# Kernel optimization log

Hardware: AMD Instinct MI355X
Metric: run time of the kernel (lower is better)

## Reference

```python
import jax, jax.numpy as jnp
import numpy as np

EPS = 1e-12
LAMBDA = 0.5  # kernel['lambda'] for the binary kernel

D, H, Z = 3072, 1024, 32
BS, NN = 128, 32


def setup_inputs() -> dict:
    key = jax.random.key(0)
    ks = jax.random.split(key, 16)
    sc = lambda fan_in: 1.0 / np.sqrt(fan_in)
    inp = {
        "x_c": jax.random.normal(ks[0], (BS, D), jnp.float32),
        "x_nn": jax.random.normal(ks[1], (BS, NN, D), jnp.float32),
        # encoder params: D -> H -> H -> Z
        "We1": jax.random.normal(ks[2], (D, H), jnp.float32) * sc(D),
        "be1": jnp.zeros((H,), jnp.float32),
        "We2": jax.random.normal(ks[3], (H, H), jnp.float32) * sc(H),
        "be2": jnp.zeros((H,), jnp.float32),
        "We3": jax.random.normal(ks[4], (H, Z), jnp.float32) * sc(H),
        "be3": jnp.zeros((Z,), jnp.float32),
        # decoder params: Z -> H -> H -> D
        "Wd1": jax.random.normal(ks[5], (Z, H), jnp.float32) * sc(Z),
        "bd1": jnp.zeros((H,), jnp.float32),
        "Wd2": jax.random.normal(ks[6], (H, H), jnp.float32) * sc(H),
        "bd2": jnp.zeros((H,), jnp.float32),
        "Wd3": jax.random.normal(ks[7], (H, D), jnp.float32) * sc(H),
        "bd3": jnp.zeros((D,), jnp.float32),
    }
    return inp


def _mlp(x, W1, b1, W2, b2, W3, b3):
    h = jax.nn.relu(x @ W1 + b1)
    h = jax.nn.relu(h @ W2 + b2)
    return h @ W3 + b3


def reference(x_c, x_nn, We1, be1, We2, be2, We3, be3,
              Wd1, bd1, Wd2, bd2, Wd3, bd3):
    bs, num_nn, dim = x_nn.shape

    enc = lambda x: _mlp(x, We1, be1, We2, be2, We3, be3)
    dec = lambda z: _mlp(z, Wd1, bd1, Wd2, bd2, Wd3, bd3)

    z_c = enc(x_c)                                   # (bs, Z)
    z_dim = z_c.shape[1]
    z_nn = enc(x_nn.reshape(-1, dim)).reshape(bs, num_nn, z_dim)

    recon = dec(z_c)                                 # (bs, D)
    dz = z_nn - z_c[:, None, :]                      # (bs, nn, Z)
    v = dz.reshape(-1, z_dim)                        # (bs*nn, Z)
    inputs = jnp.broadcast_to(z_c[:, None, :], (bs, num_nn, z_dim)).reshape(-1, z_dim)

    # approx_order == 2: Jacobian-vector and Hessian-bilinear (dz^T H dz) via nested jvp
    jac_fn = lambda z: jax.jvp(dec, (z,), (v,))[1]   # J(z) dz, (bs*nn, D)
    jac, hess = jax.jvp(jac_fn, (inputs,), (v,))     # each (bs*nn, D)

    n_recon = recon[:, None, :] + (jac + 0.5 * hess).reshape(bs, num_nn, dim)

    n_loss = jnp.sum((x_nn - n_recon) ** 2, axis=2)  # ||.||^2, (bs, nn)

    # binary kernel: 1 where neighbor differs from center, lambda where identical
    dist = jnp.linalg.norm(x_c[:, None, :] - x_nn, axis=2)
    weights = jnp.where(dist > EPS, 1.0, LAMBDA)

    loss = jnp.mean(weights * n_loss)
    return loss
```

## Files before the change

### kernel.cpp

```cpp
#include <hip/hip_runtime.h>
#include <math.h>

#define D_DIM 3072
#define H_DIM 1024
#define Z_DIM 32
#define BATCH 128
#define NNEI 32
#define NROWS (BATCH * NNEI)
#define MENC (NROWS + BATCH)

typedef __attribute__((ext_vector_type(8))) short short8;
typedef __attribute__((ext_vector_type(4))) float f32x4;
typedef unsigned short ushortT;

__device__ __forceinline__ unsigned short f2bf(float f) {
  union { float f; unsigned int u; } v; v.f = f;
  unsigned int r = v.u + 0x7FFFu + ((v.u >> 16) & 1u);
  return (unsigned short)(r >> 16);
}
__device__ __forceinline__ float bf2f(unsigned short b) {
  union { unsigned int u; float f; } v; v.u = ((unsigned int)b) << 16;
  return v.f;
}

enum { EP_RELU = 0, EP_BIAS = 1, EP_LOSS = 2 };

template <int MODE, int TN>
__global__ __launch_bounds__(256) __attribute__((amdgpu_waves_per_eu(1, 2)))
void gemm_sb(
    const ushortT* __restrict__ A, const ushortT* __restrict__ BT,
    const float* __restrict__ bias, ushortT* __restrict__ C,
    int M, int N, int K,
    const ushortT* __restrict__ xa,
    const float* __restrict__ wrow,
    float* __restrict__ out) {
  constexpr int NF = TN / 32;

  __shared__ __align__(16) ushortT As[4096];
  __shared__ __align__(16) ushortT Bs[TN * 32];

  const int t = threadIdx.x;
  const int wave = t >> 6;
  const int lane = t & 63;
  const int quad = lane >> 4;
  const int lm = lane & 15;
  const int bm = blockIdx.y * 128;
  const int bn = blockIdx.x * TN;
  const int wr = (wave >> 1) * 64;
  const int wc = (wave & 1) * (TN / 2);

  f32x4 acc[4][NF];
#pragma unroll
  for (int i = 0; i < 4; ++i)
#pragma unroll
    for (int j = 0; j < NF; ++j) acc[i][j] = (f32x4)0.f;

  const int a_r0 = (t >> 6) * 16 + (t & 15);
  const int a_q8 = ((t >> 4) & 3) * 8;
  const ushortT* ga0 = A + (size_t)(bm + a_r0) * K + a_q8;
  const ushortT* ga1 = ga0 + (size_t)64 * K;
  ushortT* wa0 = As + t * 8;
  ushortT* wa1 = As + t * 8 + 2048;

  const ushortT* gb0 = nullptr;
  const ushortT* gb1 = nullptr;
  ushortT* wb0 = nullptr;
  ushortT* wb1 = nullptr;
  bool bact = true;
  if (TN == 128) {
    gb0 = BT + (size_t)(bn + a_r0) * K + a_q8;
    gb1 = gb0 + (size_t)64 * K;
    wb0 = Bs + t * 8;
    wb1 = Bs + t * 8 + 2048;
  } else {
    bact = (t < 128);
    const int s = t & 127;
    const int b_r = (s >> 6) * 16 + (s & 15);
    const int b_q8 = ((s >> 4) & 3) * 8;
    gb0 = BT + (size_t)(bn + b_r) * K + b_q8;
    wb0 = Bs + s * 8;
  }

  uint4 ra0 = *(const uint4*)ga0;
  uint4 ra1 = *(const uint4*)ga1;
  uint4 rb0 = {0, 0, 0, 0};
  uint4 rb1 = {0, 0, 0, 0};
  if (bact) rb0 = *(const uint4*)gb0;
  if (TN == 128) rb1 = *(const uint4*)gb1;
  ga0 += 32; ga1 += 32;
  gb0 += 32;
  if (TN == 128) gb1 += 32;

  const ushortT* arp = As + (wr >> 4) * 512 + lane * 8;
  const ushortT* brp = Bs + (wc >> 4) * 512 + lane * 8;

  for (int k0 = 0; k0 < K; k0 += 32) {
    __syncthreads();
    *(uint4*)wa0 = ra0;
    *(uint4*)wa1 = ra1;
    if (bact) *(uint4*)wb0 = rb0;
    if (TN == 128) *(uint4*)wb1 = rb1;
    __syncthreads();

    if (k0 + 32 < K) {
      ra0 = *(const uint4*)ga0;
      ra1 = *(const uint4*)ga1;
      if (bact) rb0 = *(const uint4*)gb0;
      if (TN == 128) rb1 = *(const uint4*)gb1;
      ga0 += 32; ga1 += 32;
      gb0 += 32;
      if (TN == 128) gb1 += 32;
    }

    short8 af[4], bf[NF];
#pragma unroll
    for (int mt = 0; mt < 4; ++mt) af[mt] = *(const short8*)(arp + mt * 512);
#pragma unroll
    for (int nt = 0; nt < NF; ++nt) bf[nt] = *(const short8*)(brp + nt * 512);
#pragma unroll
    for (int mt = 0; mt < 4; ++mt)
#pragma unroll
      for (int nt = 0; nt < NF; ++nt)
        acc[mt][nt] = __builtin_amdgcn_mfma_f32_16x16x32_bf16(af[mt], bf[nt], acc[mt][nt], 0, 0, 0);
  }

  if (MODE == EP_LOSS) {
    __shared__ float red[256];
    float lsum = 0.f;
#pragma unroll
    for (int mt = 0; mt < 4; ++mt) {
#pragma unroll
      for (int r = 0; r < 4; ++r) {
        const int row = bm + wr + mt * 16 + quad * 4 + r;
        const float w = wrow[row];
        const ushortT* xr = xa + (size_t)row * N;
        float rs = 0.f;
#pragma unroll
        for (int nt = 0; nt < NF; ++nt) {
          const int col = bn + wc + nt * 16 + lm;
          const float d = bf2f(xr[col]) - (acc[mt][nt][r] + bias[col]);
          rs = fmaf(d, d, rs);
        }
        lsum = fmaf(w, rs, lsum);
      }
    }
    __syncthreads();
    red[t] = lsum;
    __syncthreads();
    for (int st = 128; st > 0; st >>= 1) {
      if (t < st) red[t] += red[t + st];
      __syncthreads();
    }
    if (t == 0) atomicAdd(out, red[0] * (1.0f / (float)NROWS));
  } else {
#pragma unroll
    for (int mt = 0; mt < 4; ++mt)
#pragma unroll
      for (int r = 0; r < 4; ++r) {
        const int row = bm + wr + mt * 16 + quad * 4 + r;
#pragma unroll
        for (int nt = 0; nt < NF; ++nt) {
          const int col = bn + wc + nt * 16 + lm;
          float v = acc[mt][nt][r] + bias[col];
          if (MODE == EP_RELU) v = fmaxf(v, 0.f);
          C[(size_t)row * N + col] = f2bf(v);
        }
      }
  }
}

__global__ __launch_bounds__(256) void mask_apply(
    const ushortT* __restrict__ U, ushortT* __restrict__ outp) {
  const int i4 = (blockIdx.x * 256 + threadIdx.x) * 4;
  const int r = i4 >> 10;
  const int c = i4 & 1023;
  ushort4 u = *(const ushort4*)(U + i4);
  ushort4 o;
  if (r < NROWS) {
    const ushort4 m = *(const ushort4*)(U + (((size_t)(NROWS + (r >> 5))) << 10) + c);
    o.x = ((short)m.x > 0) ? u.x : 0;
    o.y = ((short)m.y > 0) ? u.y : 0;
    o.z = ((short)m.z > 0) ? u.z : 0;
    o.w = ((short)m.w > 0) ? u.w : 0;
  } else {
    o.x = ((short)u.x > 0) ? u.x : 0;
    o.y = ((short)u.y > 0) ? u.y : 0;
    o.z = ((short)u.z > 0) ? u.z : 0;
    o.w = ((short)u.w > 0) ? u.w : 0;
  }
  *(ushort4*)(outp + i4) = o;
}

__global__ __launch_bounds__(256) void prep_kernel(
    const float* __restrict__ x_c, const float* __restrict__ x_nn,
    ushortT* __restrict__ A_enc, float* __restrict__ wbuf, float* __restrict__ out) {
  const int i = blockIdx.x;
  const int t = threadIdx.x;
  if (i < NROWS) {
    const float* src = x_nn + (size_t)i * D_DIM;
    const float* ctr = x_c + (size_t)(i >> 5) * D_DIM;
    ushortT* dst = A_enc + (size_t)i * D_DIM;
    float s = 0.f;
    for (int d = t * 4; d < D_DIM; d += 1024) {
      const float4 v = *(const float4*)(src + d);
      const float4 c = *(const float4*)(ctr + d);
      ushort4 o;
      o.x = f2bf(v.x); o.y = f2bf(v.y); o.z = f2bf(v.z); o.w = f2bf(v.w);
      *(ushort4*)(dst + d) = o;
      const float dx = v.x - c.x, dy = v.y - c.y, dz = v.z - c.z, dw = v.w - c.w;
      s += dx * dx + dy * dy + dz * dz + dw * dw;
    }
    __shared__ float red[256];
    red[t] = s;
    __syncthreads();
    for (int st = 128; st > 0; st >>= 1) {
      if (t < st) red[t] += red[t + st];
      __syncthreads();
    }
    if (t == 0) {
      wbuf[i] = (red[0] > 1e-24f) ? 1.0f : 0.5f;
      if (i == 0) out[0] = 0.f;
    }
  } else {
    const int r = i - NROWS;
    const float* src = x_c + (size_t)r * D_DIM;
    ushortT* dst = A_enc + (size_t)i * D_DIM;
    for (int d = t * 4; d < D_DIM; d += 1024) {
      const float4 v = *(const float4*)(src + d);
      ushort4 o;
      o.x = f2bf(v.x); o.y = f2bf(v.y); o.z = f2bf(v.z); o.w = f2bf(v.w);
      *(ushort4*)(dst + d) = o;
    }
  }
}

__global__ __launch_bounds__(256) void trans_all(
    const float* __restrict__ We1, const float* __restrict__ We2,
    const float* __restrict__ We3, const float* __restrict__ Wd1,
    const float* __restrict__ Wd2, const float* __restrict__ Wd3,
    ushortT* __restrict__ We1T, ushortT* __restrict__ We2T,
    ushortT* __restrict__ We3T, ushortT* __restrict__ Wd1T,
    ushortT* __restrict__ Wd2T, ushortT* __restrict__ Wd3T) {
  const int b = blockIdx.x;
  const float* W; ushortT* WT; int K, N, loc;
  if (b < 3072)      { W = We1; WT = We1T; K = 3072; N = 1024; loc = b; }
  else if (b < 4096) { W = We2; WT = We2T; K = 1024; N = 1024; loc = b - 3072; }
  else if (b < 4128) { W = We3; WT = We3T; K = 1024; N = 32;   loc = b - 4096; }
  else if (b < 4160) { W = Wd1; WT = Wd1T; K = 32;   N = 1024; loc = b - 4128; }
  else if (b < 5184) { W = Wd2; WT = Wd2T; K = 1024; N = 1024; loc = b - 4160; }
  else               { W = Wd3; WT = Wd3T; K = 1024; N = 3072; loc = b - 5184; }
  const int ntiles = N >> 5;
  const int n0 = (loc % ntiles) * 32;
  const int k0 = (loc / ntiles) * 32;
  __shared__ float tile[32][33];
  const int tx = threadIdx.x & 31;
  const int ty = threadIdx.x >> 5;
  for (int i = ty; i < 32; i += 8)
    tile[i][tx] = W[(size_t)(k0 + i) * N + n0 + tx];
  __syncthreads();
  for (int i = ty; i < 32; i += 8)
    WT[(size_t)(n0 + i) * K + k0 + tx] = f2bf(tile[tx][i]);
}

extern "C" void kernel_launch(void* const* d_in, const int* in_sizes, int n_in,
                              void* d_out, int out_size, void* d_ws, size_t ws_size,
                              hipStream_t stream) {
  const float* x_c = (const float*)d_in[0];
  const float* x_nn = (const float*)d_in[1];
  const float* We1 = (const float*)d_in[2];
  const float* be1 = (const float*)d_in[3];
  const float* We2 = (const float*)d_in[4];
  const float* be2 = (const float*)d_in[5];
  const float* We3 = (const float*)d_in[6];
  const float* be3 = (const float*)d_in[7];
  const float* Wd1 = (const float*)d_in[8];
  const float* bd1 = (const float*)d_in[9];
  const float* Wd2 = (const float*)d_in[10];
  const float* bd2 = (const float*)d_in[11];
  const float* Wd3 = (const float*)d_in[12];
  const float* bd3 = (const float*)d_in[13];
  float* out = (float*)d_out;

  char* p = (char*)d_ws;
  auto alloc = [&](size_t bytes) {
    char* r = p;
    p += (bytes + 255) & ~(size_t)255;
    return r;
  };
  ushortT* We1T = (ushortT*)alloc((size_t)H_DIM * D_DIM * 2);
  ushortT* We2T = (ushortT*)alloc((size_t)H_DIM * H_DIM * 2);
  ushortT* We3T = (ushortT*)alloc((size_t)Z_DIM * H_DIM * 2);
  ushortT* Wd1T = (ushortT*)alloc((size_t)H_DIM * Z_DIM * 2);
  ushortT* Wd2T = (ushortT*)alloc((size_t)H_DIM * H_DIM * 2);
  ushortT* Wd3T = (ushortT*)alloc((size_t)D_DIM * H_DIM * 2);
  ushortT* A_enc = (ushortT*)alloc((size_t)MENC * D_DIM * 2);
  ushortT* bufX = (ushortT*)alloc((size_t)MENC * H_DIM * 2);
  ushortT* bufY = (ushortT*)alloc((size_t)MENC * H_DIM * 2);
  ushortT* z = (ushortT*)alloc((size_t)MENC * Z_DIM * 2);
  float* wbuf = (float*)alloc((size_t)NROWS * 4);

  const dim3 blk(256);
  const float* nofp = nullptr;
  const ushortT* nobf = nullptr;

  prep_kernel<<<dim3(MENC), blk, 0, stream>>>(x_c, x_nn, A_enc, wbuf, out);
  trans_all<<<dim3(8256), blk, 0, stream>>>(We1, We2, We3, Wd1, Wd2, Wd3,
                                            We1T, We2T, We3T, Wd1T, Wd2T, Wd3T);

  gemm_sb<EP_RELU, 128><<<dim3(8, 33), blk, 0, stream>>>(
      A_enc, We1T, be1, bufX, MENC, H_DIM, D_DIM, nobf, nofp, nullptr);
  gemm_sb<EP_RELU, 128><<<dim3(8, 33), blk, 0, stream>>>(
      bufX, We2T, be2, bufY, MENC, H_DIM, H_DIM, nobf, nofp, nullptr);
  gemm_sb<EP_BIAS, 32><<<dim3(1, 33), blk, 0, stream>>>(
      bufY, We3T, be3, z, MENC, Z_DIM, H_DIM, nobf, nofp, nullptr);

  gemm_sb<EP_BIAS, 128><<<dim3(8, 33), blk, 0, stream>>>(
      z, Wd1T, bd1, bufX, MENC, H_DIM, Z_DIM, nobf, nofp, nullptr);
  mask_apply<<<dim3((MENC * H_DIM) / 1024), blk, 0, stream>>>(bufX, bufY);
  gemm_sb<EP_BIAS, 128><<<dim3(8, 33), blk, 0, stream>>>(
      bufY, Wd2T, bd2, bufX, MENC, H_DIM, H_DIM, nobf, nofp, nullptr);
  mask_apply<<<dim3((NROWS * H_DIM) / 1024), blk, 0, stream>>>(bufX, bufY);
  gemm_sb<EP_LOSS, 128><<<dim3(24, 32), blk, 0, stream>>>(
      bufY, Wd3T, bd3, nullptr, NROWS, D_DIM, H_DIM, A_enc, wbuf, out);
}
```

Baseline: 406.2 us.

## Double-buffer LDS tiles in GEMM with two-stage register prefetch

Converts the single-buffered GEMM main loop into a double-buffered one with two LDS tile slots and two sets of prefetch registers loaded two k-steps ahead. This drops one of the two barriers per k-step and lets LDS stores for the next tile overlap MFMA work on the current tile, hiding more global-load latency. The cost is doubled shared memory and more live registers, which may lower occupancy.

```diff
diff --git a/kernel.cpp b/kernel.cpp
--- a/kernel.cpp
+++ b/kernel.cpp
@@ -27,7 +27,7 @@
 
 template <int MODE, int TN>
 __global__ __launch_bounds__(256) __attribute__((amdgpu_waves_per_eu(1, 2)))
-void gemm_sb(
+void gemm_db(
     const ushortT* __restrict__ A, const ushortT* __restrict__ BT,
     const float* __restrict__ bias, ushortT* __restrict__ C,
     int M, int N, int K,
@@ -36,8 +36,8 @@
     float* __restrict__ out) {
   constexpr int NF = TN / 32;
 
-  __shared__ __align__(16) ushortT As[4096];
-  __shared__ __align__(16) ushortT Bs[TN * 32];
+  __shared__ __align__(16) ushortT As[2][4096];
+  __shared__ __align__(16) ushortT Bs[2][TN * 32];
 
   const int t = threadIdx.x;
   const int wave = t >> 6;
@@ -59,70 +59,93 @@
   const int a_q8 = ((t >> 4) & 3) * 8;
   const ushortT* ga0 = A + (size_t)(bm + a_r0) * K + a_q8;
   const ushortT* ga1 = ga0 + (size_t)64 * K;
-  ushortT* wa0 = As + t * 8;
-  ushortT* wa1 = As + t * 8 + 2048;
 
   const ushortT* gb0 = nullptr;
   const ushortT* gb1 = nullptr;
-  ushortT* wb0 = nullptr;
-  ushortT* wb1 = nullptr;
   bool bact = true;
+  int bslot = t;
   if (TN == 128) {
     gb0 = BT + (size_t)(bn + a_r0) * K + a_q8;
     gb1 = gb0 + (size_t)64 * K;
-    wb0 = Bs + t * 8;
-    wb1 = Bs + t * 8 + 2048;
   } else {
     bact = (t < 128);
-    const int s = t & 127;
-    const int b_r = (s >> 6) * 16 + (s & 15);
-    const int b_q8 = ((s >> 4) & 3) * 8;
+    bslot = t & 127;
+    const int b_r = (bslot >> 6) * 16 + (bslot & 15);
+    const int b_q8 = ((bslot >> 4) & 3) * 8;
     gb0 = BT + (size_t)(bn + b_r) * K + b_q8;
-    wb0 = Bs + s * 8;
-  }
-
-  uint4 ra0 = *(const uint4*)ga0;
-  uint4 ra1 = *(const uint4*)ga1;
-  uint4 rb0 = {0, 0, 0, 0};
-  uint4 rb1 = {0, 0, 0, 0};
-  if (bact) rb0 = *(const uint4*)gb0;
-  if (TN == 128) rb1 = *(const uint4*)gb1;
-  ga0 += 32; ga1 += 32;
-  gb0 += 32;
-  if (TN == 128) gb1 += 32;
-
-  const ushortT* arp = As + (wr >> 4) * 512 + lane * 8;
-  const ushortT* brp = Bs + (wc >> 4) * 512 + lane * 8;
-
-  for (int k0 = 0; k0 < K; k0 += 32) {
-    __syncthreads();
-    *(uint4*)wa0 = ra0;
-    *(uint4*)wa1 = ra1;
-    if (bact) *(uint4*)wb0 = rb0;
-    if (TN == 128) *(uint4*)wb1 = rb1;
-    __syncthreads();
-
-    if (k0 + 32 < K) {
-      ra0 = *(const uint4*)ga0;
-      ra1 = *(const uint4*)ga1;
-      if (bact) rb0 = *(const uint4*)gb0;
-      if (TN == 128) rb1 = *(const uint4*)gb1;
-      ga0 += 32; ga1 += 32;
-      gb0 += 32;
-      if (TN == 128) gb1 += 32;
-    }
-
-    short8 af[4], bf[NF];
-#pragma unroll
-    for (int mt = 0; mt < 4; ++mt) af[mt] = *(const short8*)(arp + mt * 512);
-#pragma unroll
-    for (int nt = 0; nt < NF; ++nt) bf[nt] = *(const short8*)(brp + nt * 512);
-#pragma unroll
-    for (int mt = 0; mt < 4; ++mt)
-#pragma unroll
-      for (int nt = 0; nt < NF; ++nt)
-        acc[mt][nt] = __builtin_amdgcn_mfma_f32_16x16x32_bf16(af[mt], bf[nt], acc[mt][nt], 0, 0, 0);
-  }
+  }
+
+#define LDA(r0, r1, kk)                                   \
+  {                                                       \
+    r0 = *(const uint4*)(ga0 + (size_t)(kk) * 32);        \
+    r1 = *(const uint4*)(ga1 + (size_t)(kk) * 32);        \
+  }
+#define LDB(r0, r1, kk)                                   \
+  {                                                       \
+    if (TN == 128) {                                      \
+      r0 = *(const uint4*)(gb0 + (size_t)(kk) * 32);      \
+      r1 = *(const uint4*)(gb1 + (size_t)(kk) * 32);      \
+    } else if (bact) {                                    \
+      r0 = *(const uint4*)(gb0 + (size_t)(kk) * 32);      \
+    }                                                     \
+  }
+#define STW(bsel, A0, A1, B0, B1)                         \
+  {                                                       \
+    *(uint4*)&As[bsel][t * 8] = A0;                       \
+    *(uint4*)&As[bsel][t * 8 + 2048] = A1;                \
+    if (TN == 128) {                                      \
+      *(uint4*)&Bs[bsel][t * 8] = B0;                     \
+      *(uint4*)&Bs[bsel][t * 8 + 2048] = B1;              \
+    } else if (bact) {                                    \
+      *(uint4*)&Bs[bsel][bslot * 8] = B0;                 \
+    }                                                     \
+  }
+#define CMP(bsel)                                                           \
+  {                                                                         \
+    const ushortT* arp = &As[bsel][(wr >> 4) * 512 + lane * 8];             \
+    const ushortT* brp = &Bs[bsel][(wc >> 4) * 512 + lane * 8];             \
+    short8 af[4], bf[NF];                                                   \
+    _Pragma("unroll") for (int mt = 0; mt < 4; ++mt)                        \
+        af[mt] = *(const short8*)(arp + mt * 512);                          \
+    _Pragma("unroll") for (int nt = 0; nt < NF; ++nt)                       \
+        bf[nt] = *(const short8*)(brp + nt * 512);                          \
+    _Pragma("unroll") for (int mt = 0; mt < 4; ++mt)                        \
+        _Pragma("unroll") for (int nt = 0; nt < NF; ++nt)                   \
+            acc[mt][nt] = __builtin_amdgcn_mfma_f32_16x16x32_bf16(          \
+                af[mt], bf[nt], acc[mt][nt], 0, 0, 0);                      \
+  }
+
+  const int nk = K / 32;
+  uint4 ea0, ea1, eb0 = {0, 0, 0, 0}, eb1 = {0, 0, 0, 0};
+  uint4 oa0 = {0, 0, 0, 0}, oa1 = {0, 0, 0, 0};
+  uint4 ob0 = {0, 0, 0, 0}, ob1 = {0, 0, 0, 0};
+
+  LDA(ea0, ea1, 0); LDB(eb0, eb1, 0);
+  if (nk > 1) { LDA(oa0, oa1, 1); LDB(ob0, ob1, 1); }
+  STW(0, ea0, ea1, eb0, eb1);
+  if (nk > 2) { LDA(ea0, ea1, 2); LDB(eb0, eb1, 2); }
+  __syncthreads();
+
+  for (int k = 0; k < nk; k += 2) {
+    if (k + 1 < nk) {
+      STW(1, oa0, oa1, ob0, ob1);
+      if (k + 3 < nk) { LDA(oa0, oa1, k + 3); LDB(ob0, ob1, k + 3); }
+    }
+    CMP(0);
+    if (k + 1 < nk) {
+      __syncthreads();
+      if (k + 2 < nk) {
+        STW(0, ea0, ea1, eb0, eb1);
+        if (k + 4 < nk) { LDA(ea0, ea1, k + 4); LDB(eb0, eb1, k + 4); }
+      }
+      CMP(1);
+      if (k + 2 < nk) __syncthreads();
+    }
+  }
+#undef LDA
+#undef LDB
+#undef STW
+#undef CMP
 
   if (MODE == EP_LOSS) {
     __shared__ float red[256];
@@ -307,19 +330,19 @@
   trans_all<<<dim3(8256), blk, 0, stream>>>(We1, We2, We3, Wd1, Wd2, Wd3,
                                             We1T, We2T, We3T, Wd1T, Wd2T, Wd3T);
 
-  gemm_sb<EP_RELU, 128><<<dim3(8, 33), blk, 0, stream>>>(
+  gemm_db<EP_RELU, 128><<<dim3(8, 33), blk, 0, stream>>>(
       A_enc, We1T, be1, bufX, MENC, H_DIM, D_DIM, nobf, nofp, nullptr);
-  gemm_sb<EP_RELU, 128><<<dim3(8, 33), blk, 0, stream>>>(
+  gemm_db<EP_RELU, 128><<<dim3(8, 33), blk, 0, stream>>>(
       bufX, We2T, be2, bufY, MENC, H_DIM, H_DIM, nobf, nofp, nullptr);
-  gemm_sb<EP_BIAS, 32><<<dim3(1, 33), blk, 0, stream>>>(
+  gemm_db<EP_BIAS, 32><<<dim3(1, 33), blk, 0, stream>>>(
       bufY, We3T, be3, z, MENC, Z_DIM, H_DIM, nobf, nofp, nullptr);
 
-  gemm_sb<EP_BIAS, 128><<<dim3(8, 33), blk, 0, stream>>>(
+  gemm_db<EP_BIAS, 128><<<dim3(8, 33), blk, 0, stream>>>(
       z, Wd1T, bd1, bufX, MENC, H_DIM, Z_DIM, nobf, nofp, nullptr);
   mask_apply<<<dim3((MENC * H_DIM) / 1024), blk, 0, stream>>>(bufX, bufY);
-  gemm_sb<EP_BIAS, 128><<<dim3(8, 33), blk, 0, stream>>>(
+  gemm_db<EP_BIAS, 128><<<dim3(8, 33), blk, 0, stream>>>(
       bufY, Wd2T, bd2, bufX, MENC, H_DIM, H_DIM, nobf, nofp, nullptr);
   mask_apply<<<dim3((NROWS * H_DIM) / 1024), blk, 0, stream>>>(bufX, bufY);
-  gemm_sb<EP_LOSS, 128><<<dim3(24, 32), blk, 0, stream>>>(
+  gemm_db<EP_LOSS, 128><<<dim3(24, 32), blk, 0, stream>>>(
       bufY, Wd3T, bd3, nullptr, NROWS, D_DIM, H_DIM, A_enc, wbuf, out);
 }
```

After: 403.4 us. Within noise of the previous version (-0.7%).

## Use 64-deep K tiles for big GEMMs and split-K for the narrow encoder output

Applied to the files above, without the earlier changes.

Adds a gemm64 kernel that stages 64-wide K slices per iteration, halving the number of barrier pairs per GEMM, and uses it for the large encoder and decoder GEMMs. The narrow H->Z encoder GEMM, which previously launched only 33 blocks, now splits K eight ways, writes fp32 partials, and reduces them with bias in a separate kernel. The aim is fewer synchronisations per unit of MFMA work and better occupancy on the small GEMM, at the cost of doubled LDS per block and an extra partial-sum buffer and launch.

```diff
diff --git a/kernel.cpp b/kernel.cpp
--- a/kernel.cpp
+++ b/kernel.cpp
@@ -23,7 +23,171 @@
   return v.f;
 }
 
-enum { EP_RELU = 0, EP_BIAS = 1, EP_LOSS = 2 };
+enum { EP_RELU = 0, EP_BIAS = 1, EP_PART = 2, EP_LOSS = 3 };
+
+template <int MODE, int TN>
+__global__ __launch_bounds__(256) __attribute__((amdgpu_waves_per_eu(1, 2)))
+void gemm64(
+    const ushortT* __restrict__ A, const ushortT* __restrict__ BT,
+    const float* __restrict__ bias, ushortT* __restrict__ C,
+    float* __restrict__ P, int M, int N, int K, int Ks,
+    const ushortT* __restrict__ xa,
+    const float* __restrict__ wrow,
+    float* __restrict__ out) {
+  constexpr int NF = TN / 32;
+
+  __shared__ __align__(16) ushortT As[8192];
+  __shared__ __align__(16) ushortT Bs[TN * 64];
+
+  const int t = threadIdx.x;
+  const int wave = t >> 6;
+  const int lane = t & 63;
+  const int quad = lane >> 4;
+  const int lm = lane & 15;
+  const int bm = blockIdx.y * 128;
+  const int bn = blockIdx.x * TN;
+  const int koff = blockIdx.z * Ks;
+  const int wr = (wave >> 1) * 64;
+  const int wc = (wave & 1) * (TN / 2);
+
+  f32x4 acc[4][NF];
+#pragma unroll
+  for (int i = 0; i < 4; ++i)
+#pragma unroll
+    for (int j = 0; j < NF; ++j) acc[i][j] = (f32x4)0.f;
+
+  const int a_r0 = (t >> 6) * 16 + (t & 15);
+  const int a_q8 = ((t >> 4) & 3) * 8;
+  const ushortT* ga = A + (size_t)(bm + a_r0) * K + koff + a_q8;
+  const size_t aK64 = (size_t)64 * K;
+
+  const ushortT* gb = nullptr;
+  if (TN == 128) {
+    gb = BT + (size_t)(bn + a_r0) * K + koff + a_q8;
+  } else {
+    const int b_r = ((t >> 6) & 1) * 16 + (t & 15);
+    const int b_k = (t >> 7) * 32 + ((t >> 4) & 3) * 8;
+    gb = BT + (size_t)(bn + b_r) * K + koff + b_k;
+  }
+
+  uint4 a0, a1, a2, a3, b0, b1 = {0,0,0,0}, b2 = {0,0,0,0}, b3 = {0,0,0,0};
+
+#define LOADT(kk)                                               \
+  {                                                             \
+    const size_t o = (size_t)(kk) * 64;                         \
+    a0 = *(const uint4*)(ga + o);                               \
+    a1 = *(const uint4*)(ga + aK64 + o);                        \
+    a2 = *(const uint4*)(ga + o + 32);                          \
+    a3 = *(const uint4*)(ga + aK64 + o + 32);                   \
+    b0 = *(const uint4*)(gb + o);                               \
+    if (TN == 128) {                                            \
+      b1 = *(const uint4*)(gb + aK64 + o);                      \
+      b2 = *(const uint4*)(gb + o + 32);                        \
+      b3 = *(const uint4*)(gb + aK64 + o + 32);                 \
+    }                                                           \
+  }
+#define STORET()                                                \
+  {                                                             \
+    *(uint4*)&As[t * 8] = a0;                                   \
+    *(uint4*)&As[t * 8 + 2048] = a1;                            \
+    *(uint4*)&As[t * 8 + 4096] = a2;                            \
+    *(uint4*)&As[t * 8 + 6144] = a3;                            \
+    if (TN == 128) {                                            \
+      *(uint4*)&Bs[t * 8] = b0;                                 \
+      *(uint4*)&Bs[t * 8 + 2048] = b1;                          \
+      *(uint4*)&Bs[t * 8 + 4096] = b2;                          \
+      *(uint4*)&Bs[t * 8 + 6144] = b3;                          \
+    } else {                                                    \
+      *(uint4*)&Bs[t * 8] = b0;                                 \
+    }                                                           \
+  }
+
+  const int nk = Ks / 64;
+  LOADT(0);
+
+  for (int k0 = 0; k0 < nk; ++k0) {
+    __syncthreads();
+    STORET();
+    __syncthreads();
+    if (k0 + 1 < nk) LOADT(k0 + 1);
+
+#pragma unroll
+    for (int kk = 0; kk < 2; ++kk) {
+      const ushortT* arp = &As[kk * 4096 + (wr >> 4) * 512 + lane * 8];
+      const ushortT* brp = (TN == 128)
+          ? &Bs[kk * 4096 + (wc >> 4) * 512 + lane * 8]
+          : &Bs[kk * 1024 + (wc >> 4) * 512 + lane * 8];
+      short8 af[4], bf[NF];
+#pragma unroll
+      for (int mt = 0; mt < 4; ++mt) af[mt] = *(const short8*)(arp + mt * 512);
+#pragma unroll
+      for (int nt = 0; nt < NF; ++nt) bf[nt] = *(const short8*)(brp + nt * 512);
+#pragma unroll
+      for (int mt = 0; mt < 4; ++mt)
+#pragma unroll
+        for (int nt = 0; nt < NF; ++nt)
+          acc[mt][nt] = __builtin_amdgcn_mfma_f32_16x16x32_bf16(af[mt], bf[nt], acc[mt][nt], 0, 0, 0);
+    }
+  }
+#undef LOADT
+#undef STORET
+
+  if (MODE == EP_LOSS) {
+    __shared__ float red[256];
+    float lsum = 0.f;
+#pragma unroll
+    for (int mt = 0; mt < 4; ++mt) {
+#pragma unroll
+      for (int r = 0; r < 4; ++r) {
+        const int row = bm + wr + mt * 16 + quad * 4 + r;
+        const float w = wrow[row];
+        const ushortT* xr = xa + (size_t)row * N;
+        float rs = 0.f;
+#pragma unroll
+        for (int nt = 0; nt < NF; ++nt) {
+          const int col = bn + wc + nt * 16 + lm;
+          const float d = bf2f(xr[col]) - (acc[mt][nt][r] + bias[col]);
+          rs = fmaf(d, d, rs);
+        }
+        lsum = fmaf(w, rs, lsum);
+      }
+    }
+    __syncthreads();
+    red[t] = lsum;
+    __syncthreads();
+    for (int st = 128; st > 0; st >>= 1) {
+      if (t < st) red[t] += red[t + st];
+      __syncthreads();
+    }
+    if (t == 0) atomicAdd(out, red[0] * (1.0f / (float)NROWS));
+  } else if (MODE == EP_PART) {
+#pragma unroll
+    for (int mt = 0; mt < 4; ++mt)
+#pragma unroll
+      for (int r = 0; r < 4; ++r) {
+        const int row = bm + wr + mt * 16 + quad * 4 + r;
+#pragma unroll
+        for (int nt = 0; nt < NF; ++nt) {
+          const int col = bn + wc + nt * 16 + lm;
+          P[((size_t)blockIdx.z * M + row) * N + col] = acc[mt][nt][r];
+        }
+      }
+  } else {
+#pragma unroll
+    for (int mt = 0; mt < 4; ++mt)
+#pragma unroll
+      for (int r = 0; r < 4; ++r) {
+        const int row = bm + wr + mt * 16 + quad * 4 + r;
+#pragma unroll
+        for (int nt = 0; nt < NF; ++nt) {
+          const int col = bn + wc + nt * 16 + lm;
+          float v = acc[mt][nt][r] + bias[col];
+          if (MODE == EP_RELU) v = fmaxf(v, 0.f);
+          C[(size_t)row * N + col] = f2bf(v);
+        }
+      }
+  }
+}
 
 template <int MODE, int TN>
 __global__ __launch_bounds__(256) __attribute__((amdgpu_waves_per_eu(1, 2)))
@@ -31,11 +195,9 @@
     const ushortT* __restrict__ A, const ushortT* __restrict__ BT,
     const float* __restrict__ bias, ushortT* __restrict__ C,
     int M, int N, int K,
-    const ushortT* __restrict__ xa,
-    const float* __restrict__ wrow,
+    const ushortT* __restrict__ xa, const float* __restrict__ wrow,
     float* __restrict__ out) {
   constexpr int NF = TN / 32;
-
   __shared__ __align__(16) ushortT As[4096];
   __shared__ __align__(16) ushortT Bs[TN * 32];
 
@@ -59,59 +221,32 @@
   const int a_q8 = ((t >> 4) & 3) * 8;
   const ushortT* ga0 = A + (size_t)(bm + a_r0) * K + a_q8;
   const ushortT* ga1 = ga0 + (size_t)64 * K;
-  ushortT* wa0 = As + t * 8;
-  ushortT* wa1 = As + t * 8 + 2048;
-
-  const ushortT* gb0 = nullptr;
-  const ushortT* gb1 = nullptr;
-  ushortT* wb0 = nullptr;
-  ushortT* wb1 = nullptr;
-  bool bact = true;
-  if (TN == 128) {
-    gb0 = BT + (size_t)(bn + a_r0) * K + a_q8;
-    gb1 = gb0 + (size_t)64 * K;
-    wb0 = Bs + t * 8;
-    wb1 = Bs + t * 8 + 2048;
-  } else {
-    bact = (t < 128);
-    const int s = t & 127;
-    const int b_r = (s >> 6) * 16 + (s & 15);
-    const int b_q8 = ((s >> 4) & 3) * 8;
-    gb0 = BT + (size_t)(bn + b_r) * K + b_q8;
-    wb0 = Bs + s * 8;
-  }
+  const ushortT* gb0 = BT + (size_t)(bn + a_r0) * K + a_q8;
+  const ushortT* gb1 = gb0 + (size_t)64 * K;
 
   uint4 ra0 = *(const uint4*)ga0;
   uint4 ra1 = *(const uint4*)ga1;
-  uint4 rb0 = {0, 0, 0, 0};
-  uint4 rb1 = {0, 0, 0, 0};
-  if (bact) rb0 = *(const uint4*)gb0;
-  if (TN == 128) rb1 = *(const uint4*)gb1;
-  ga0 += 32; ga1 += 32;
-  gb0 += 32;
-  if (TN == 128) gb1 += 32;
+  uint4 rb0 = *(const uint4*)gb0;
+  uint4 rb1 = *(const uint4*)gb1;
+  ga0 += 32; ga1 += 32; gb0 += 32; gb1 += 32;
 
   const ushortT* arp = As + (wr >> 4) * 512 + lane * 8;
   const ushortT* brp = Bs + (wc >> 4) * 512 + lane * 8;
 
   for (int k0 = 0; k0 < K; k0 += 32) {
     __syncthreads();
-    *(uint4*)wa0 = ra0;
-    *(uint4*)wa1 = ra1;
-    if (bact) *(uint4*)wb0 = rb0;
-    if (TN == 128) *(uint4*)wb1 = rb1;
-    __syncthreads();
-
+    *(uint4*)&As[t * 8] = ra0;
+    *(uint4*)&As[t * 8 + 2048] = ra1;
+    *(uint4*)&Bs[t * 8] = rb0;
+    *(uint4*)&Bs[t * 8 + 2048] = rb1;
+    __syncthreads();
     if (k0 + 32 < K) {
       ra0 = *(const uint4*)ga0;
       ra1 = *(const uint4*)ga1;
-      if (bact) rb0 = *(const uint4*)gb0;
-      if (TN == 128) rb1 = *(const uint4*)gb1;
-      ga0 += 32; ga1 += 32;
-      gb0 += 32;
-      if (TN == 128) gb1 += 32;
-    }
-
+      rb0 = *(const uint4*)gb0;
+      rb1 = *(const uint4*)gb1;
+      ga0 += 32; ga1 += 32; gb0 += 32; gb1 += 32;
+    }
     short8 af[4], bf[NF];
 #pragma unroll
     for (int mt = 0; mt < 4; ++mt) af[mt] = *(const short8*)(arp + mt * 512);
@@ -124,49 +259,38 @@
         acc[mt][nt] = __builtin_amdgcn_mfma_f32_16x16x32_bf16(af[mt], bf[nt], acc[mt][nt], 0, 0, 0);
   }
 
-  if (MODE == EP_LOSS) {
-    __shared__ float red[256];
-    float lsum = 0.f;
-#pragma unroll
-    for (int mt = 0; mt < 4; ++mt) {
-#pragma unroll
-      for (int r = 0; r < 4; ++r) {
-        const int row = bm + wr + mt * 16 + quad * 4 + r;
-        const float w = wrow[row];
-        const ushortT* xr = xa + (size_t)row * N;
-        float rs = 0.f;
-#pragma unroll
-        for (int nt = 0; nt < NF; ++nt) {
-          const int col = bn + wc + nt * 16 + lm;
-          const float d = bf2f(xr[col]) - (acc[mt][nt][r] + bias[col]);
-          rs = fmaf(d, d, rs);
-        }
-        lsum = fmaf(w, rs, lsum);
+#pragma unroll
+  for (int mt = 0; mt < 4; ++mt)
+#pragma unroll
+    for (int r = 0; r < 4; ++r) {
+      const int row = bm + wr + mt * 16 + quad * 4 + r;
+#pragma unroll
+      for (int nt = 0; nt < NF; ++nt) {
+        const int col = bn + wc + nt * 16 + lm;
+        float v = acc[mt][nt][r] + bias[col];
+        if (MODE == EP_RELU) v = fmaxf(v, 0.f);
+        C[(size_t)row * N + col] = f2bf(v);
       }
     }
-    __syncthreads();
-    red[t] = lsum;
-    __syncthreads();
-    for (int st = 128; st > 0; st >>= 1) {
-      if (t < st) red[t] += red[t + st];
-      __syncthreads();
-    }
-    if (t == 0) atomicAdd(out, red[0] * (1.0f / (float)NROWS));
-  } else {
-#pragma unroll
-    for (int mt = 0; mt < 4; ++mt)
-#pragma unroll
-      for (int r = 0; r < 4; ++r) {
-        const int row = bm + wr + mt * 16 + quad * 4 + r;
-#pragma unroll
-        for (int nt = 0; nt < NF; ++nt) {
-          const int col = bn + wc + nt * 16 + lm;
-          float v = acc[mt][nt][r] + bias[col];
-          if (MODE == EP_RELU) v = fmaxf(v, 0.f);
-          C[(size_t)row * N + col] = f2bf(v);
-        }
-      }
-  }
+}
+
+template <int S>
+__global__ __launch_bounds__(256) void reduce_lin(
+    const float* __restrict__ P, const float* __restrict__ bias,
+    ushortT* __restrict__ outp, int MN, int Nmask) {
+  const int i4 = (blockIdx.x * 256 + threadIdx.x) * 4;
+  if (i4 >= MN) return;
+  float4 s = *(const float4*)(P + i4);
+#pragma unroll
+  for (int k = 1; k < S; ++k) {
+    const float4 q = *(const float4*)(P + (size_t)k * MN + i4);
+    s.x += q.x; s.y += q.y; s.z += q.z; s.w += q.w;
+  }
+  const float4 b = *(const float4*)(bias + (i4 & Nmask));
+  ushort4 o;
+  o.x = f2bf(s.x + b.x); o.y = f2bf(s.y + b.y);
+  o.z = f2bf(s.z + b.z); o.w = f2bf(s.w + b.w);
+  *(ushort4*)(outp + i4) = o;
 }
 
 __global__ __launch_bounds__(256) void mask_apply(
@@ -297,6 +421,7 @@
   ushortT* bufX = (ushortT*)alloc((size_t)MENC * H_DIM * 2);
   ushortT* bufY = (ushortT*)alloc((size_t)MENC * H_DIM * 2);
   ushortT* z = (ushortT*)alloc((size_t)MENC * Z_DIM * 2);
+  float* Pz = (float*)alloc((size_t)8 * MENC * Z_DIM * 4);
   float* wbuf = (float*)alloc((size_t)NROWS * 4);
 
   const dim3 blk(256);
@@ -307,19 +432,21 @@
   trans_all<<<dim3(8256), blk, 0, stream>>>(We1, We2, We3, Wd1, Wd2, Wd3,
                                             We1T, We2T, We3T, Wd1T, Wd2T, Wd3T);
 
-  gemm_sb<EP_RELU, 128><<<dim3(8, 33), blk, 0, stream>>>(
-      A_enc, We1T, be1, bufX, MENC, H_DIM, D_DIM, nobf, nofp, nullptr);
-  gemm_sb<EP_RELU, 128><<<dim3(8, 33), blk, 0, stream>>>(
-      bufX, We2T, be2, bufY, MENC, H_DIM, H_DIM, nobf, nofp, nullptr);
-  gemm_sb<EP_BIAS, 32><<<dim3(1, 33), blk, 0, stream>>>(
-      bufY, We3T, be3, z, MENC, Z_DIM, H_DIM, nobf, nofp, nullptr);
+  gemm64<EP_RELU, 128><<<dim3(8, 33, 1), blk, 0, stream>>>(
+      A_enc, We1T, be1, bufX, nullptr, MENC, H_DIM, D_DIM, D_DIM, nobf, nofp, nullptr);
+  gemm64<EP_RELU, 128><<<dim3(8, 33, 1), blk, 0, stream>>>(
+      bufX, We2T, be2, bufY, nullptr, MENC, H_DIM, H_DIM, H_DIM, nobf, nofp, nullptr);
+  gemm64<EP_PART, 32><<<dim3(1, 33, 8), blk, 0, stream>>>(
+      bufY, We3T, nofp, nullptr, Pz, MENC, Z_DIM, H_DIM, H_DIM / 8, nobf, nofp, nullptr);
+  reduce_lin<8><<<dim3((MENC * Z_DIM) / 1024), blk, 0, stream>>>(
+      Pz, be3, z, MENC * Z_DIM, Z_DIM - 1);
 
   gemm_sb<EP_BIAS, 128><<<dim3(8, 33), blk, 0, stream>>>(
       z, Wd1T, bd1, bufX, MENC, H_DIM, Z_DIM, nobf, nofp, nullptr);
   mask_apply<<<dim3((MENC * H_DIM) / 1024), blk, 0, stream>>>(bufX, bufY);
-  gemm_sb<EP_BIAS, 128><<<dim3(8, 33), blk, 0, stream>>>(
-      bufY, Wd2T, bd2, bufX, MENC, H_DIM, H_DIM, nobf, nofp, nullptr);
+  gemm64<EP_BIAS, 128><<<dim3(8, 33, 1), blk, 0, stream>>>(
+      bufY, Wd2T, bd2, bufX, nullptr, MENC, H_DIM, H_DIM, H_DIM, nobf, nofp, nullptr);
   mask_apply<<<dim3((NROWS * H_DIM) / 1024), blk, 0, stream>>>(bufX, bufY);
-  gemm_sb<EP_LOSS, 128><<<dim3(24, 32), blk, 0, stream>>>(
-      bufY, Wd3T, bd3, nullptr, NROWS, D_DIM, H_DIM, A_enc, wbuf, out);
-}
+  gemm64<EP_LOSS, 128><<<dim3(24, 32, 1), blk, 0, stream>>>(
+      bufY, Wd3T, bd3, nullptr, nullptr, NROWS, D_DIM, H_DIM, H_DIM, A_enc, wbuf, out);
+}
```

Result: faster. 389.1 us (-4.2%).
